# Performance work log

Hardware: AMD Instinct MI355X
Metric: run time of the kernel (lower is better)

The kernel has to match this reference:

```python
import jax, jax.numpy as jnp
import numpy as np

T, B, E = 1024, 4, 1024
H = 16
D = E // H          # head_dim = 64
L = 16              # max_relative_length


def setup_inputs() -> dict:
    key = jax.random.key(0)
    ks = jax.random.split(key, 4)
    query = jax.random.normal(ks[0], (T, B, E), dtype=jnp.float32)
    # xavier-ish scaled params
    in_proj_weight = jax.random.normal(ks[1], (3 * E, E), dtype=jnp.float32) * (1.0 / np.sqrt(E))
    in_proj_bias = jnp.zeros((3 * E,), dtype=jnp.float32)
    rel_pos_keys = jax.random.normal(ks[2], (2 * L + 1, E), dtype=jnp.float32) * (1.0 / np.sqrt(E))
    out_w = jax.random.normal(ks[3], (E, E), dtype=jnp.float32) * (1.0 / np.sqrt(E))
    out_b = jnp.zeros((E,), dtype=jnp.float32)
    return {"query": query, "in_proj_weight": in_proj_weight, "in_proj_bias": in_proj_bias,
            "rel_pos_keys": rel_pos_keys, "out_w": out_w, "out_b": out_b}


def reference(query, in_proj_weight, in_proj_bias, rel_pos_keys, out_w, out_b):
    t, b, e = query.shape
    scaling = D ** (-0.5)
    # fused qkv projection: [T,B,3E]
    qkv = jnp.einsum('tbe,fe->tbf', query, in_proj_weight) + in_proj_bias
    q, k, v = jnp.split(qkv, 3, axis=-1)
    q = q * scaling
    # [T,B,E] -> [B*H, T, D]
    def heads(x):
        return x.reshape(t, b * H, D).transpose(1, 0, 2)
    q, k, v = heads(q), heads(k), heads(v)
    # clipped relative position matrix [T,T] in [0, 2L]
    r = jnp.arange(t)
    dist = jnp.clip(r[None, :] - r[:, None], -L, L) + L
    # gather relation keys, keep first head_dim channels: [T,T,D]
    rel_k = rel_pos_keys[dist][:, :, :D]
    # scores = q k^T + q . rel_k  (Shaw et al.), [B*H, T, T]
    scores = jnp.einsum('btd,bsd->bts', q, k) + jnp.einsum('btd,tsd->bts', q, rel_k)
    probs = jax.nn.softmax(scores, axis=-1)
    attn = jnp.einsum('bts,bsd->btd', probs, v)      # [B*H, T, D]
    attn = attn.transpose(1, 0, 2).reshape(t, b, e)   # [T, B, E]
    return jnp.einsum('tbe,oe->tbo', attn, out_w) + out_b
```

## Files before the change

### kernel.cpp

```cpp
#include <hip/hip_runtime.h>
#include <hip/hip_bf16.h>

typedef __attribute__((ext_vector_type(8))) short short8;
typedef __attribute__((ext_vector_type(4))) float floatx4;


__device__ __forceinline__ short f2bf(float x) {
  union { float f; unsigned u; } cv; cv.f = x;
  unsigned u = cv.u + (0x7FFFu + ((cv.u >> 16) & 1u));
  return (short)(u >> 16);
}

__device__ __forceinline__ unsigned pk_bf16(float a, float b) {
  union { __hip_bfloat162 h; unsigned u; } cv;
  cv.h = __float22bfloat162_rn(make_float2(a, b));
  return cv.u;
}

__device__ __forceinline__ floatx4 mfma16(short8 a, short8 b, floatx4 c) {
  return __builtin_amdgcn_mfma_f32_16x16x32_bf16(a, b, c, 0, 0, 0);
}

__device__ __forceinline__ void async_copy16(const void* g, void* l) {
  __builtin_amdgcn_global_load_lds((const __attribute__((address_space(1))) void*)g,
                                   (__attribute__((address_space(3))) void*)l, 16, 0, 0);
}

__global__ void __launch_bounds__(256) convert_all_kernel(
    const float* __restrict__ s0, const float* __restrict__ s1,
    const float* __restrict__ s2,
    short* __restrict__ d0, short* __restrict__ d1, short* __restrict__ d2)
{
  int i = blockIdx.x * 256 + threadIdx.x;
  if (i < 524288) {
    int e8 = i & 127, b = (i >> 7) & 3, t = i >> 9;
    const float4* s = (const float4*)s0 + (size_t)i * 2;
    float4 a = s[0], c = s[1];
    uint4 o = make_uint4(pk_bf16(a.x, a.y), pk_bf16(a.z, a.w),
                         pk_bf16(c.x, c.y), pk_bf16(c.z, c.w));
    *(uint4*)(d0 + (size_t)b * 1048576 + t * 1024 + e8 * 8) = o;
  } else {
    const float* src; short* dst; int off;
    if (i < 917504) { src = s1; dst = d1; off = i - 524288; }
    else            { src = s2; dst = d2; off = i - 917504; }
    const float4* s = (const float4*)src + (size_t)off * 2;
    float4 a = s[0], c = s[1];
    uint4 o = make_uint4(pk_bf16(a.x, a.y), pk_bf16(a.z, a.w),
                         pk_bf16(c.x, c.y), pk_bf16(c.z, c.w));
    *(uint4*)(dst + (size_t)off * 8) = o;
  }
}

__device__ __forceinline__ void gemm_stage(
    const short* __restrict__ A, const short* __restrict__ W,
    short* Atile, short* Btile, int m0, int n0, int K, int kk, int tid, int w)
{
  #pragma unroll
  for (int i = 0; i < 2; i++) {
    int seg = i * 256 + tid;
    int row = seg >> 2, p = seg & 3;
    int ck = (p - ((row >> 1) & 3)) & 3;
    async_copy16(A + (size_t)(m0 + row) * K + kk + ck * 8,
                 Atile + (size_t)(i * 256 + w * 64) * 8);
    async_copy16(W + (size_t)(n0 + row) * K + kk + ck * 8,
                 Btile + (size_t)(i * 256 + w * 64) * 8);
  }
}

__device__ __forceinline__ void gemm_core_db(
    const short* __restrict__ A, const short* __restrict__ W,
    short* At, short* Bt,
    int m0, int n0, int K, int tid, floatx4 acc[4][4])
{
  const int lane = tid & 63, w = tid >> 6;
  const int quad = lane >> 4, l16 = lane & 15;
  const int wm = (w >> 1) * 64, wn = (w & 1) * 64;
  #pragma unroll
  for (int mt = 0; mt < 4; mt++)
    #pragma unroll
    for (int nt = 0; nt < 4; nt++) acc[mt][nt] = (floatx4)(0.0f);

  gemm_stage(A, W, At, Bt, m0, n0, K, 0, tid, w);

  for (int kk = 0; kk < K; kk += 32) {
    const int cur = (kk >> 5) & 1;
    short* Ac = At + cur * (128 * 32);
    short* Bc = Bt + cur * (128 * 32);
    __syncthreads();
    if (kk + 32 < K)
      gemm_stage(A, W, At + (1 - cur) * (128 * 32), Bt + (1 - cur) * (128 * 32),
                 m0, n0, K, kk + 32, tid, w);
    short8 af[4], bfr[4];
    #pragma unroll
    for (int mt = 0; mt < 4; mt++) {
      int R = wm + mt * 16 + l16;
      af[mt] = *(const short8*)(Ac + R * 32 + ((quad + (R >> 1)) & 3) * 8);
    }
    #pragma unroll
    for (int nt = 0; nt < 4; nt++) {
      int R = wn + nt * 16 + l16;
      bfr[nt] = *(const short8*)(Bc + R * 32 + ((quad + (R >> 1)) & 3) * 8);
    }
    #pragma unroll
    for (int mt = 0; mt < 4; mt++)
      #pragma unroll
      for (int nt = 0; nt < 4; nt++)
        acc[mt][nt] = mfma16(af[mt], bfr[nt], acc[mt][nt]);
  }
}

__global__ void __launch_bounds__(256) gemm_qkv(
    const short* __restrict__ A, const short* __restrict__ W,
    const float* __restrict__ bias,
    short* __restrict__ q_ws, short* __restrict__ k_ws, short* __restrict__ v_ws)
{
  __shared__ __align__(16) short Atile[2 * 128 * 32];
  __shared__ __align__(16) short Btile[2 * 128 * 32];
  const int tid = threadIdx.x;
  const int m0 = blockIdx.x * 128, n0 = blockIdx.y * 128;
  floatx4 acc[4][4];
  gemm_core_db(A, W, Atile, Btile, m0, n0, 1024, tid, acc);

  const int lane = tid & 63, w = tid >> 6;
  const int quad = lane >> 4, l16 = lane & 15;
  const int wm = (w >> 1) * 64, wn = (w & 1) * 64;
  const int which = n0 >> 10;
  #pragma unroll
  for (int nt = 0; nt < 4; nt++) {
    int f = n0 + wn + nt * 16 + l16;
    float bv = bias[f];
    int h = (f >> 6) & 15;
    int d = f & 63;
    if (which == 2) {
      #pragma unroll
      for (int mt = 0; mt < 4; mt++) {
        int r0 = m0 + wm + mt * 16 + quad * 4;
        int t = r0 & 1023, bb = r0 >> 10;
        int bh = bb * 16 + h;
        unsigned lo = pk_bf16(acc[mt][nt][0] + bv, acc[mt][nt][1] + bv);
        unsigned hi = pk_bf16(acc[mt][nt][2] + bv, acc[mt][nt][3] + bv);
        *(uint2*)(v_ws + ((size_t)bh * 64 + d) * 1024 + t) = make_uint2(lo, hi);
      }
    } else {
      short* dst = which ? k_ws : q_ws;
      const float sc = which ? 1.0f : 0.125f;
      #pragma unroll
      for (int mt = 0; mt < 4; mt++) {
        int r0 = m0 + wm + mt * 16 + quad * 4;
        int t = r0 & 1023, bb = r0 >> 10;
        int bh = bb * 16 + h;
        unsigned u01 = pk_bf16((acc[mt][nt][0] + bv) * sc, (acc[mt][nt][1] + bv) * sc);
        unsigned u23 = pk_bf16((acc[mt][nt][2] + bv) * sc, (acc[mt][nt][3] + bv) * sc);
        size_t base = ((size_t)bh * 1024 + t) * 64 + d;
        dst[base]           = (short)u01;
        dst[base + 64]      = (short)(u01 >> 16);
        dst[base + 128]     = (short)u23;
        dst[base + 192]     = (short)(u23 >> 16);
      }
    }
  }
}

__global__ void __launch_bounds__(256) attn_kernel(
    const short* __restrict__ q_ws, const short* __restrict__ k_ws,
    const short* __restrict__ v_ws, const float* __restrict__ relk,
    short* __restrict__ attn_ws)
{
  __shared__ float rel_lds[128 * 33];
  __shared__ __align__(16) short Ktile[64 * 64];
  __shared__ __align__(16) short Vtile[64 * 64];
  __shared__ __align__(16) short p_lds[4][32 * 64];
  const int tid = threadIdx.x, lane = tid & 63, w = tid >> 6;
  const int quad = lane >> 4, l16 = lane & 15;
  const int bh = 8 * ((int)blockIdx.x & 7) + (((int)blockIdx.x >> 3) & 7);
  const int t0 = ((int)blockIdx.x >> 6) * 128;
  const int b = bh >> 4, h = bh & 15;

  short8 aq[2][2];
  #pragma unroll
  for (int qt = 0; qt < 2; qt++)
    #pragma unroll
    for (int ks = 0; ks < 2; ks++)
      aq[qt][ks] = *(const short8*)(q_ws
          + ((size_t)bh * 1024 + t0 + qt * 64 + w * 16 + l16) * 64
          + ks * 32 + quad * 8);

  for (int i = tid; i < 48 * 8; i += 256) {
    int row = i >> 3, p = i & 7;
    short8 val;
    if (row < 33) {
      const float* src = relk + row * 1024 + p * 8;
      float4 a = *(const float4*)src, c = *(const float4*)(src + 4);
      val[0] = f2bf(a.x); val[1] = f2bf(a.y); val[2] = f2bf(a.z); val[3] = f2bf(a.w);
      val[4] = f2bf(c.x); val[5] = f2bf(c.y); val[6] = f2bf(c.z); val[7] = f2bf(c.w);
    } else {
      val = (short8)0;
    }
    *(short8*)(Ktile + row * 64 + ((p ^ (row & 7)) << 3)) = val;
  }
  __syncthreads();

  #pragma unroll
  for (int qt = 0; qt < 2; qt++) {
    #pragma unroll
    for (int jt = 0; jt < 3; jt++) {
      floatx4 scR = (floatx4)(0.0f);
      #pragma unroll
      for (int ks = 0; ks < 2; ks++) {
        int rrow = jt * 16 + l16;
        int ck = (quad + 4 * ks) ^ (rrow & 7);
        short8 rb = *(const short8*)(Ktile + rrow * 64 + ck * 8);
        scR = mfma16(aq[qt][ks], rb, scR);
      }
      int j = jt * 16 + l16;
      if (j < 33) {
        #pragma unroll
        for (int reg = 0; reg < 4; reg++) {
          int tl = qt * 64 + w * 16 + quad * 4 + reg;
          rel_lds[tl * 33 + j] = scR[reg];
        }
      }
    }
  }
  __syncthreads();

  float biasLo[2], biasHi[2];
  #pragma unroll
  for (int qt = 0; qt < 2; qt++) {
    int ql = qt * 64 + w * 16 + l16;
    biasLo[qt] = rel_lds[ql * 33 + 0];
    biasHi[qt] = rel_lds[ql * 33 + 32];
  }

  floatx4 o[2][4];
  #pragma unroll
  for (int qt = 0; qt < 2; qt++)
    #pragma unroll
    for (int dt = 0; dt < 4; dt++) o[qt][dt] = (floatx4)(0.0f);
  float rsum[2] = {0.f, 0.f};

  const short* kg = k_ws + (size_t)bh * 1024 * 64;
  const short* vg = v_ws + (size_t)bh * 64 * 1024;

  for (int st = 0; st < 16; st++) {
    const int s0 = st * 64;
    #pragma unroll
    for (int i = 0; i < 2; i++) {
      int seg = i * 256 + tid;
      int row = seg >> 3, p = seg & 7;
      int ck = p ^ (row & 7);
      async_copy16(kg + (size_t)(s0 + row) * 64 + ck * 8,
                   Ktile + (size_t)(i * 256 + w * 64) * 8);
      async_copy16(vg + (size_t)row * 1024 + s0 + ck * 8,
                   Vtile + (size_t)(i * 256 + w * 64) * 8);
    }
    __syncthreads();

    short8 kb[4][2];
    #pragma unroll
    for (int nt = 0; nt < 4; nt++)
      #pragma unroll
      for (int ks = 0; ks < 2; ks++) {
        int srow = nt * 16 + l16;
        kb[nt][ks] = *(const short8*)(Ktile + srow * 64
                                      + (((quad + 4 * ks) ^ (l16 & 7)) << 3));
      }

    floatx4 sc[2][4];
    #pragma unroll
    for (int qt = 0; qt < 2; qt++)
      #pragma unroll
      for (int nt = 0; nt < 4; nt++) {
        sc[qt][nt] = (floatx4)(0.0f);
        #pragma unroll
        for (int ks = 0; ks < 2; ks++)
          sc[qt][nt] = mfma16(kb[nt][ks], aq[qt][ks], sc[qt][nt]);
      }

    #pragma unroll
    for (int qt = 0; qt < 2; qt++) {
      const int qbase = t0 + qt * 64 + w * 16;
      bool alllo = (s0 <= qbase - 79);
      bool allhi = (s0 >= qbase + 31);
      if (alllo || allhi) {
        float bb = alllo ? biasLo[qt] : biasHi[qt];
        #pragma unroll
        for (int nt = 0; nt < 4; nt++)
          #pragma unroll
          for (int reg = 0; reg < 4; reg++) sc[qt][nt][reg] += bb;
      } else {
        int ql = qt * 64 + w * 16 + l16;
        #pragma unroll
        for (int nt = 0; nt < 4; nt++)
          #pragma unroll
          for (int reg = 0; reg < 4; reg++) {
            int delta = (s0 + 16 * nt + 4 * quad + reg) - (qbase + l16);
            delta = min(max(delta, -16), 16) + 16;
            sc[qt][nt][reg] += rel_lds[ql * 33 + delta];
          }
      }
      #pragma unroll
      for (int nt = 0; nt < 4; nt++) {
        #pragma unroll
        for (int reg = 0; reg < 4; reg++) {
          float p = __expf(sc[qt][nt][reg]);
          sc[qt][nt][reg] = p;
          rsum[qt] += p;
        }
        unsigned w0 = pk_bf16(sc[qt][nt][0], sc[qt][nt][1]);
        unsigned w1 = pk_bf16(sc[qt][nt][2], sc[qt][nt][3]);
        int srot = (16 * nt + 4 * quad + 4 * l16) & 63;
        *(uint2*)(p_lds[w] + (qt * 16 + l16) * 64 + srot) = make_uint2(w0, w1);
      }
    }

    short8 ap[2][2];
    #pragma unroll
    for (int qt = 0; qt < 2; qt++)
      #pragma unroll
      for (int ks = 0; ks < 2; ks++) {
        int s1 = (32 * ks + 8 * quad + 4 * l16) & 63;
        int s2 = (s1 + 4) & 63;
        union { short8 v; uint2 u[2]; } pu;
        pu.u[0] = *(const uint2*)(p_lds[w] + (qt * 16 + l16) * 64 + s1);
        pu.u[1] = *(const uint2*)(p_lds[w] + (qt * 16 + l16) * 64 + s2);
        ap[qt][ks] = pu.v;
      }

    #pragma unroll
    for (int dt = 0; dt < 4; dt++) {
      short8 vb[2];
      #pragma unroll
      for (int ks = 0; ks < 2; ks++) {
        int drow = dt * 16 + l16;
        vb[ks] = *(const short8*)(Vtile + drow * 64
                                  + (((quad + 4 * ks) ^ (l16 & 7)) << 3));
      }
      #pragma unroll
      for (int qt = 0; qt < 2; qt++)
        #pragma unroll
        for (int ks = 0; ks < 2; ks++)
          o[qt][dt] = mfma16(ap[qt][ks], vb[ks], o[qt][dt]);
    }
    __syncthreads();
  }

  #pragma unroll
  for (int qt = 0; qt < 2; qt++) {
    float rs = rsum[qt];
    rs += __shfl_xor(rs, 16, 64);
    rs += __shfl_xor(rs, 32, 64);
    float inv[4];
    #pragma unroll
    for (int reg = 0; reg < 4; reg++)
      inv[reg] = 1.0f / __shfl(rs, quad * 4 + reg, 64);
    #pragma unroll
    for (int dt = 0; dt < 4; dt++) {
      unsigned u01 = pk_bf16(o[qt][dt][0] * inv[0], o[qt][dt][1] * inv[1]);
      unsigned u23 = pk_bf16(o[qt][dt][2] * inv[2], o[qt][dt][3] * inv[3]);
      int tg = t0 + qt * 64 + w * 16 + quad * 4;
      size_t base = ((size_t)tg * 4 + b) * 1024 + h * 64 + dt * 16 + l16;
      attn_ws[base]         = (short)u01;
      attn_ws[base + 4096]  = (short)(u01 >> 16);
      attn_ws[base + 8192]  = (short)u23;
      attn_ws[base + 12288] = (short)(u23 >> 16);
    }
  }
}

__global__ void __launch_bounds__(256) gemm_outproj(
    const short* __restrict__ A, const short* __restrict__ W,
    const float* __restrict__ bias, float* __restrict__ out)
{
  __shared__ __align__(16) short Atile[2 * 64 * 32];
  __shared__ __align__(16) short Btile[2 * 128 * 32];
  const int tid = threadIdx.x;
  const int m0 = blockIdx.x * 64, n0 = blockIdx.y * 128;
  const int lane = tid & 63, w = tid >> 6;
  const int quad = lane >> 4, l16 = lane & 15;
  const int wm = (w >> 1) * 32, wn = (w & 1) * 64;

  floatx4 acc[2][4];
  #pragma unroll
  for (int mt = 0; mt < 2; mt++)
    #pragma unroll
    for (int nt = 0; nt < 4; nt++) acc[mt][nt] = (floatx4)(0.0f);

  #define STAGE_OP(KK, BUF)                                                  \
    {                                                                        \
      _Pragma("unroll")                                                      \
      for (int i = 0; i < 2; i++) {                                          \
        int seg = i * 256 + tid;                \
        int row = seg >> 2, p = seg & 3;                                     \
        int ck = (p - ((row >> 1) & 3)) & 3;                                 \
        async_copy16(W + (size_t)(n0 + row) * 1024 + (KK) + ck * 8,          \
                     Btile + (size_t)((BUF) * 4096 + (i * 256 + w * 64) * 8)); \
      }                                                                      \
      {                                                                      \
        int row = tid >> 2, p = tid & 3;         \
        int ck = (p - ((row >> 1) & 3)) & 3;                                 \
        async_copy16(A + (size_t)(m0 + row) * 1024 + (KK) + ck * 8,          \
                     Atile + (size_t)((BUF) * 2048 + (w * 64) * 8));         \
      }                                                                      \
    }

  STAGE_OP(0, 0);
  for (int kk = 0; kk < 1024; kk += 32) {
    const int cur = (kk >> 5) & 1;
    const short* Ac = Atile + cur * 2048;
    const short* Bc = Btile + cur * 4096;
    __syncthreads();
    if (kk + 32 < 1024) STAGE_OP(kk + 32, 1 - cur);
    short8 af[2], bfr[4];
    #pragma unroll
    for (int mt = 0; mt < 2; mt++) {
      int R = wm + mt * 16 + l16;
      af[mt] = *(const short8*)(Ac + R * 32 + ((quad + (R >> 1)) & 3) * 8);
    }
    #pragma unroll
    for (int nt = 0; nt < 4; nt++) {
      int R = wn + nt * 16 + l16;
      bfr[nt] = *(const short8*)(Bc + R * 32 + ((quad + (R >> 1)) & 3) * 8);
    }
    #pragma unroll
    for (int mt = 0; mt < 2; mt++)
      #pragma unroll
      for (int nt = 0; nt < 4; nt++)
        acc[mt][nt] = mfma16(af[mt], bfr[nt], acc[mt][nt]);
  }
  #undef STAGE_OP

  #pragma unroll
  for (int nt = 0; nt < 4; nt++) {
    int f = n0 + wn + nt * 16 + l16;
    float bv = bias[f];
    #pragma unroll
    for (int mt = 0; mt < 2; mt++) {
      #pragma unroll
      for (int reg = 0; reg < 4; reg++) {
        int r = m0 + wm + mt * 16 + quad * 4 + reg;
        out[(size_t)r * 1024 + f] = acc[mt][nt][reg] + bv;
      }
    }
  }
}

extern "C" void kernel_launch(void* const* d_in, const int* in_sizes, int n_in,
                              void* d_out, int out_size, void* d_ws, size_t ws_size,
                              hipStream_t stream) {
  const float* query = (const float*)d_in[0];
  const float* in_w  = (const float*)d_in[1];
  const float* in_b  = (const float*)d_in[2];
  const float* relk  = (const float*)d_in[3];
  const float* out_w = (const float*)d_in[4];
  const float* out_b = (const float*)d_in[5];
  float* out = (float*)d_out;

  short* qry_bf = (short*)d_ws;
  short* win_bf = qry_bf + (size_t)4096 * 1024;
  short* wout_bf = win_bf + (size_t)3072 * 1024;
  short* q_ws   = wout_bf + (size_t)1024 * 1024;
  short* k_ws   = q_ws + (size_t)64 * 1024 * 64;
  short* v_ws   = k_ws + (size_t)64 * 1024 * 64;
  short* att_ws = v_ws + (size_t)64 * 1024 * 64;

  convert_all_kernel<<<4096, 256, 0, stream>>>(query, in_w, out_w,
                                               qry_bf, win_bf, wout_bf);
  gemm_qkv<<<dim3(32, 24), 256, 0, stream>>>(qry_bf, win_bf, in_b, q_ws, k_ws, v_ws);
  attn_kernel<<<512, 256, 0, stream>>>(q_ws, k_ws, v_ws, relk, att_ws);
  gemm_outproj<<<dim3(64, 8), 256, 0, stream>>>(att_ws, wout_bf, out_b, out);
}
```

Baseline: 177.1 us.

## Double-buffer K/V tiles in attention and use hardware exp2 with folded log2e

The attention loop now keeps two K/V shared-memory buffers. It issues the async global-to-LDS copy of the next 64-key tile right after the barrier, so those loads overlap with the current tile's math, and it drops the trailing barrier to leave one sync per iteration. Separately, log2(e) is folded into the Q scaling so softmax can call the hardware exp2 builtin instead of __expf. This removes a multiply per score. The relative-position scores come from the same scaled Q, so they stay consistent. The cost is double the K/V LDS footprint, which may reduce occupancy.

```diff
diff --git a/kernel.cpp b/kernel.cpp
--- a/kernel.cpp
+++ b/kernel.cpp
@@ -4,6 +4,8 @@
 typedef __attribute__((ext_vector_type(8))) short short8;
 typedef __attribute__((ext_vector_type(4))) float floatx4;
 
+
+#define QSCALE 0.18033688011112043f
 
 __device__ __forceinline__ short f2bf(float x) {
   union { float f; unsigned u; } cv; cv.f = x;
@@ -15,6 +17,10 @@
   union { __hip_bfloat162 h; unsigned u; } cv;
   cv.h = __float22bfloat162_rn(make_float2(a, b));
   return cv.u;
+}
+
+__device__ __forceinline__ float exp2_hw(float x) {
+  return __builtin_amdgcn_exp2f(x);
 }
 
 __device__ __forceinline__ floatx4 mfma16(short8 a, short8 b, floatx4 c) {
@@ -143,7 +149,7 @@
       }
     } else {
       short* dst = which ? k_ws : q_ws;
-      const float sc = which ? 1.0f : 0.125f;
+      const float sc = which ? 1.0f : QSCALE;
       #pragma unroll
       for (int mt = 0; mt < 4; mt++) {
         int r0 = m0 + wm + mt * 16 + quad * 4;
@@ -167,8 +173,8 @@
     short* __restrict__ attn_ws)
 {
   __shared__ float rel_lds[128 * 33];
-  __shared__ __align__(16) short Ktile[64 * 64];
-  __shared__ __align__(16) short Vtile[64 * 64];
+  __shared__ __align__(16) short Ktile[2][64 * 64];
+  __shared__ __align__(16) short Vtile[2][64 * 64];
   __shared__ __align__(16) short p_lds[4][32 * 64];
   const int tid = threadIdx.x, lane = tid & 63, w = tid >> 6;
   const int quad = lane >> 4, l16 = lane & 15;
@@ -196,7 +202,7 @@
     } else {
       val = (short8)0;
     }
-    *(short8*)(Ktile + row * 64 + ((p ^ (row & 7)) << 3)) = val;
+    *(short8*)(Ktile[0] + row * 64 + ((p ^ (row & 7)) << 3)) = val;
   }
   __syncthreads();
 
@@ -209,7 +215,7 @@
       for (int ks = 0; ks < 2; ks++) {
         int rrow = jt * 16 + l16;
         int ck = (quad + 4 * ks) ^ (rrow & 7);
-        short8 rb = *(const short8*)(Ktile + rrow * 64 + ck * 8);
+        short8 rb = *(const short8*)(Ktile[0] + rrow * 64 + ck * 8);
         scR = mfma16(aq[qt][ks], rb, scR);
       }
       int j = jt * 16 + l16;
@@ -242,19 +248,27 @@
   const short* kg = k_ws + (size_t)bh * 1024 * 64;
   const short* vg = v_ws + (size_t)bh * 64 * 1024;
 
+  #define STAGE_KV(S0, BUF)                                                  \
+    {                                                                        \
+      _Pragma("unroll")                                                      \
+      for (int i = 0; i < 2; i++) {                                          \
+        int seg = i * 256 + tid;                                             \
+        int row = seg >> 3, p = seg & 7;                                     \
+        int ck = p ^ (row & 7);                                              \
+        async_copy16(kg + (size_t)((S0) + row) * 64 + ck * 8,                \
+                     Ktile[BUF] + (size_t)(i * 256 + w * 64) * 8);           \
+        async_copy16(vg + (size_t)row * 1024 + (S0) + ck * 8,                \
+                     Vtile[BUF] + (size_t)(i * 256 + w * 64) * 8);           \
+      }                                                                      \
+    }
+
+  STAGE_KV(0, 0);
+
   for (int st = 0; st < 16; st++) {
     const int s0 = st * 64;
-    #pragma unroll
-    for (int i = 0; i < 2; i++) {
-      int seg = i * 256 + tid;
-      int row = seg >> 3, p = seg & 7;
-      int ck = p ^ (row & 7);
-      async_copy16(kg + (size_t)(s0 + row) * 64 + ck * 8,
-                   Ktile + (size_t)(i * 256 + w * 64) * 8);
-      async_copy16(vg + (size_t)row * 1024 + s0 + ck * 8,
-                   Vtile + (size_t)(i * 256 + w * 64) * 8);
-    }
+    const int cur = st & 1;
     __syncthreads();
+    if (st < 15) STAGE_KV(s0 + 64, 1 - cur);
 
     short8 kb[4][2];
     #pragma unroll
@@ -262,7 +276,7 @@
       #pragma unroll
       for (int ks = 0; ks < 2; ks++) {
         int srow = nt * 16 + l16;
-        kb[nt][ks] = *(const short8*)(Ktile + srow * 64
+        kb[nt][ks] = *(const short8*)(Ktile[cur] + srow * 64
                                       + (((quad + 4 * ks) ^ (l16 & 7)) << 3));
       }
 
@@ -303,7 +317,7 @@
       for (int nt = 0; nt < 4; nt++) {
         #pragma unroll
         for (int reg = 0; reg < 4; reg++) {
-          float p = __expf(sc[qt][nt][reg]);
+          float p = exp2_hw(sc[qt][nt][reg]);
           sc[qt][nt][reg] = p;
           rsum[qt] += p;
         }
@@ -333,7 +347,7 @@
       #pragma unroll
       for (int ks = 0; ks < 2; ks++) {
         int drow = dt * 16 + l16;
-        vb[ks] = *(const short8*)(Vtile + drow * 64
+        vb[ks] = *(const short8*)(Vtile[cur] + drow * 64
                                   + (((quad + 4 * ks) ^ (l16 & 7)) << 3));
       }
       #pragma unroll
@@ -342,8 +356,8 @@
         for (int ks = 0; ks < 2; ks++)
           o[qt][dt] = mfma16(ap[qt][ks], vb[ks], o[qt][dt]);
     }
-    __syncthreads();
-  }
+  }
+  #undef STAGE_KV
 
   #pragma unroll
   for (int qt = 0; qt < 2; qt++) {
```

Result: no change. 176.2 us (-0.5%).
